# Kernel tuning notes

Hardware: AMD Instinct MI355X
Metric: run time of the kernel (lower is better)

Reference implementation:

```python
import jax, jax.numpy as jnp
import numpy as np

B, T, D, H = 1, 2048, 1024, 16
HS = D // H  # 64
FF = 4 * D   # 4096
EPS = 1e-6


def rmsnorm(x, w):
    xf = x.astype(jnp.float32)
    n = xf * jax.lax.rsqrt(jnp.mean(xf * xf, axis=-1, keepdims=True) + EPS)
    return n.astype(x.dtype) * w


def setup_inputs() -> dict:
    key = jax.random.key(0)
    ks = jax.random.split(key, 9)
    s = 0.02
    return {
        "x": jax.random.normal(ks[0], (B, T, D), jnp.float32),
        "Wq": jax.random.normal(ks[1], (H, D, HS), jnp.float32) * s,
        "Wk": jax.random.normal(ks[2], (H, D, HS), jnp.float32) * s,
        "Wv": jax.random.normal(ks[3], (H, D, HS), jnp.float32) * s,
        "Wproj": jax.random.normal(ks[4], (H * HS, D), jnp.float32) * s,
        "bproj": jnp.zeros((D,), jnp.float32),
        "W1": jax.random.normal(ks[5], (D, FF), jnp.float32) * s,
        "W2": jax.random.normal(ks[6], (FF, D), jnp.float32) * s,
        "g1": jnp.ones((D,), jnp.float32),
        "g2": jnp.ones((D,), jnp.float32),
    }


def reference(x, Wq, Wk, Wv, Wproj, bproj, W1, W2, g1, g2):
    # --- self attention on RMSNorm(x) ---
    xn = rmsnorm(x, g1)                                   # [B,T,D]
    q = jnp.einsum('btd,hds->bhts', xn, Wq)               # [B,H,T,hs]
    k = jnp.einsum('btd,hds->bhts', xn, Wk)
    v = jnp.einsum('btd,hds->bhts', xn, Wv)
    scale = HS ** -0.5
    wei = jnp.einsum('bhts,bhus->bhtu', q, k) * scale     # [B,H,T,T]
    causal = jnp.tril(jnp.ones((T, T), bool))
    wei = jnp.where(causal, wei, -jnp.inf)
    wei = jax.nn.softmax(wei, axis=-1)
    attn = jnp.einsum('bhtu,bhus->bhts', wei, v)          # [B,H,T,hs]
    attn = attn.transpose(0, 2, 1, 3).reshape(B, T, H * HS)
    sa = attn @ Wproj + bproj                             # [B,T,D]
    x = x + sa
    # --- SiLU FFN on RMSNorm(x) ---
    xn2 = rmsnorm(x, g2)
    h = jax.nn.silu(xn2 @ W1)                             # [B,T,4D]
    x = x + h @ W2
    return x
```

## Files before the change

### kernel.cpp

```cpp
#include <hip/hip_runtime.h>

typedef unsigned short u16;
typedef unsigned int u32;
typedef __attribute__((ext_vector_type(4))) float f32x4;
typedef __attribute__((ext_vector_type(8))) __bf16 bf16x8;

#define T_SEQ 2048
#define DMODEL 1024
#define NHEAD 16
#define HEADS 64
#define FFDIM 4096
#define MNQ 2097152l

__device__ __forceinline__ u16 f2bf(float f) {
  u32 u = __builtin_bit_cast(u32, f);
  u = u + 0x7FFFu + ((u >> 16) & 1u);
  return (u16)(u >> 16);
}
__device__ __forceinline__ float bf2f(u16 h) {
  u32 u = ((u32)h) << 16;
  return __builtin_bit_cast(float, u);
}
__device__ __forceinline__ void gload_lds16(const u16* g, u16* l) {
  __builtin_amdgcn_global_load_lds(
      (const __attribute__((address_space(1))) u32*)g,
      (__attribute__((address_space(3))) u32*)l, 16, 0, 0);
}

__global__ __launch_bounds__(256) void prep_k(
    const float* __restrict__ Wq, const float* __restrict__ Wk,
    const float* __restrict__ Wv, const float* __restrict__ Wproj,
    const float* __restrict__ W1, const float* __restrict__ W2,
    const float* __restrict__ x, const float* __restrict__ g1,
    u16* __restrict__ QKVwT, u16* __restrict__ WprojT,
    u16* __restrict__ W1T, u16* __restrict__ W2T, u16* __restrict__ xn1) {
  __shared__ u16 tile[64 * 66];
  __shared__ float wsum[4];
  int bid = blockIdx.x;
  int tid = threadIdx.x;
  if (bid >= 3072) {
    int row = bid - 3072;
    const float4* xr = (const float4*)(x + (long)row * DMODEL);
    float4 v = xr[tid];
    float ss = v.x * v.x + v.y * v.y + v.z * v.z + v.w * v.w;
#pragma unroll
    for (int off = 32; off >= 1; off >>= 1) ss += __shfl_xor(ss, off, 64);
    if ((tid & 63) == 0) wsum[tid >> 6] = ss;
    __syncthreads();
    float tot = wsum[0] + wsum[1] + wsum[2] + wsum[3];
    float rms = rsqrtf(tot * (1.0f / DMODEL) + 1e-6f);
    float4 gv = ((const float4*)g1)[tid];
    ushort4 o4 = make_ushort4(f2bf(v.x * rms * gv.x), f2bf(v.y * rms * gv.y),
                              f2bf(v.z * rms * gv.z), f2bf(v.w * rms * gv.w));
    ((ushort4*)(xn1 + (long)row * DMODEL))[tid] = o4;
    return;
  }
  const float* in;
  u16* out;
  long ldin, ldout;
  int r0, c0;
  if (bid < 768) {
    int z = bid >> 4, xi = bid & 15;
    int wsel = z >> 4, h = z & 15;
    in = (wsel == 0 ? Wq : (wsel == 1 ? Wk : Wv)) + (long)h * 65536;
    out = QKVwT + (long)wsel * 1048576 + (long)h * 65536;
    ldin = 64; ldout = 1024;
    r0 = xi * 64; c0 = 0;
  } else if (bid < 1024) {
    int b = bid - 768;
    in = Wproj; out = WprojT; ldin = 1024; ldout = 1024;
    r0 = (b >> 4) * 64; c0 = (b & 15) * 64;
  } else if (bid < 2048) {
    int b = bid - 1024;
    in = W1; out = W1T; ldin = 4096; ldout = 1024;
    r0 = (b & 15) * 64; c0 = (b >> 4) * 64;
  } else {
    int b = bid - 2048;
    in = W2; out = W2T; ldin = 1024; ldout = 4096;
    r0 = (b >> 4) * 64; c0 = (b & 15) * 64;
  }
#pragma unroll
  for (int p = 0; p < 16; ++p) {
    int idx = p * 256 + tid;
    int r = idx >> 6, c = idx & 63;
    tile[c * 66 + r] = f2bf(in[(long)(r0 + r) * ldin + c0 + c]);
  }
  __syncthreads();
#pragma unroll
  for (int p = 0; p < 16; ++p) {
    int idx = p * 256 + tid;
    int c = idx >> 6, r = idx & 63;
    out[(long)(c0 + c) * ldout + r0 + r] = tile[c * 66 + r];
  }
}

__global__ __launch_bounds__(256) void proj_rms_k(
    const u16* __restrict__ part, const float* __restrict__ bias,
    const float* __restrict__ resid, const float* __restrict__ g,
    float* __restrict__ x1, u16* __restrict__ xn2) {
  int row = blockIdx.x;
  int tid = threadIdx.x;
  long i = (long)row * DMODEL + tid * 4;
  float4 r = *(const float4*)(resid + i);
  float4 bi = *(const float4*)(bias + tid * 4);
  float4 v;
  v.x = r.x + bi.x; v.y = r.y + bi.y; v.z = r.z + bi.z; v.w = r.w + bi.w;
#pragma unroll
  for (int z = 0; z < 2; ++z) {
    ushort4 a = *(const ushort4*)(part + z * MNQ + i);
    v.x += bf2f(a.x); v.y += bf2f(a.y); v.z += bf2f(a.z); v.w += bf2f(a.w);
  }
  *(float4*)(x1 + i) = v;
  float ss = v.x * v.x + v.y * v.y + v.z * v.z + v.w * v.w;
#pragma unroll
  for (int off = 32; off >= 1; off >>= 1) ss += __shfl_xor(ss, off, 64);
  __shared__ float wsum[4];
  if ((tid & 63) == 0) wsum[tid >> 6] = ss;
  __syncthreads();
  float tot = wsum[0] + wsum[1] + wsum[2] + wsum[3];
  float rms = rsqrtf(tot * (1.0f / DMODEL) + 1e-6f);
  float4 gv = ((const float4*)g)[tid];
  ushort4 o4 = make_ushort4(f2bf(v.x * rms * gv.x), f2bf(v.y * rms * gv.y),
                            f2bf(v.z * rms * gv.z), f2bf(v.w * rms * gv.w));
  ((ushort4*)(xn2 + (long)row * DMODEL))[tid] = o4;
}

template <int EPI, int MODE, int NITER>
__global__ __launch_bounds__(256, 3) void gemm_bt_k(
    const u16* __restrict__ A, const u16* __restrict__ Bt, int N,
    u16* __restrict__ out16, u16* __restrict__ vt,
    u16* __restrict__ p0, u16* __restrict__ p1) {
  __shared__ __align__(16) u16 As[3][128 * 32];
  __shared__ __align__(16) u16 Bs[3][128 * 32];
  const int K = 1024 * ((EPI == 4 && MODE == 1) ? 4 : 1);
  const int kc = NITER * 32;
  int tid = threadIdx.x;
  int w = tid >> 6, lane = tid & 63;
  int quad = lane >> 4, l15 = lane & 15;
  int wr = w >> 1, wc = w & 1;

  int bid = blockIdx.x;
  int xcd = bid & 7, s = bid >> 3;
  int nn = N >> 7;
  int bx, by, kz;
  if (MODE == 0) {
    int nl = nn >> 3;
    by = xcd * nl + s % nl;
    int r = s / nl;
    bx = r & 15;
    kz = r >> 4;
  } else {
    bx = xcd * 2 + (s & 1);
    int r = s >> 1;
    by = r % nn;
    kz = r / nn;
  }
  int m0 = bx * 128, n0 = by * 128;

  f32x4 acc[4][4] = {};

  int lr = lane >> 2;
  int sw = (lr >> 1) & 3;
  int lc = ((lane & 3) ^ sw) * 8;
  const u16* Ak = A + (long)(m0 + w * 32 + lr) * K + lc + (long)kz * kc;
  const u16* A2k = Ak + (long)16 * K;
  const u16* Bk = Bt + (long)(n0 + w * 32 + lr) * K + lc + (long)kz * kc;
  const u16* B2k = Bk + (long)16 * K;

  gload_lds16(Ak, As[0] + w * 1024);
  gload_lds16(A2k, As[0] + w * 1024 + 512);
  gload_lds16(Bk, Bs[0] + w * 1024);
  gload_lds16(B2k, Bs[0] + w * 1024 + 512);
  gload_lds16(Ak + 32, As[1] + w * 1024);
  gload_lds16(A2k + 32, As[1] + w * 1024 + 512);
  gload_lds16(Bk + 32, Bs[1] + w * 1024);
  gload_lds16(B2k + 32, Bs[1] + w * 1024 + 512);

  int swq = (l15 >> 1) & 3;
  int qoff = (quad ^ swq) << 3;

#pragma unroll
  for (int k = 0; k < NITER; ++k) {
    const int cb = k % 3;
    if (k + 2 < NITER) {
      asm volatile("s_waitcnt vmcnt(4)\n\ts_barrier" ::: "memory");
      const int pb = (k + 2) % 3;
      const int off = (k + 2) * 32;
      gload_lds16(Ak + off, As[pb] + w * 1024);
      gload_lds16(A2k + off, As[pb] + w * 1024 + 512);
      gload_lds16(Bk + off, Bs[pb] + w * 1024);
      gload_lds16(B2k + off, Bs[pb] + w * 1024 + 512);
    } else {
      asm volatile("s_waitcnt vmcnt(0)\n\ts_barrier" ::: "memory");
    }
    const u16* Ab = As[cb];
    const u16* Bb = Bs[cb];
    bf16x8 af[4], bfr[4];
#pragma unroll
    for (int mt = 0; mt < 4; ++mt)
      af[mt] = *(const bf16x8*)(Ab + (wr * 64 + mt * 16 + l15) * 32 + qoff);
#pragma unroll
    for (int nt = 0; nt < 4; ++nt)
      bfr[nt] = *(const bf16x8*)(Bb + (wc * 64 + nt * 16 + l15) * 32 + qoff);
#pragma unroll
    for (int mt = 0; mt < 4; ++mt)
#pragma unroll
      for (int nt = 0; nt < 4; ++nt)
        acc[mt][nt] = __builtin_amdgcn_mfma_f32_16x16x32_bf16(
            af[mt], bfr[nt], acc[mt][nt], 0, 0, 0);
  }

  bool vblock = (EPI == 0) && (vt != nullptr) && (n0 >= 2048);
  u16* pb = nullptr;
  if (EPI == 4) pb = (kz < 4 ? p0 : p1) + (long)(kz & 3) * MNQ;
#pragma unroll
  for (int mt = 0; mt < 4; ++mt)
#pragma unroll
    for (int nt = 0; nt < 4; ++nt) {
      int col = n0 + wc * 64 + nt * 16 + l15;
      if (EPI == 0 && vblock) {
        int sc = col - 2048;
        int row0 = m0 + wr * 64 + mt * 16 + quad * 4;
        ushort4 pk = make_ushort4(f2bf(acc[mt][nt][0]), f2bf(acc[mt][nt][1]),
                                  f2bf(acc[mt][nt][2]), f2bf(acc[mt][nt][3]));
        *(ushort4*)(vt + (long)sc * 2048 + row0) = pk;
        continue;
      }
#pragma unroll
      for (int r = 0; r < 4; ++r) {
        int row = m0 + wr * 64 + mt * 16 + quad * 4 + r;
        long idx = (long)row * N + col;
        float v = acc[mt][nt][r];
        if (EPI == 0) {
          out16[idx] = f2bf(v);
        } else if (EPI == 2) {
          out16[idx] = f2bf(v / (1.0f + __expf(-v)));
        } else if (EPI == 4) {
          pb[idx] = f2bf(v);
        }
      }
    }
}

__global__ __launch_bounds__(256) void reduce_ffn2_k(
    const u16* __restrict__ p0, const u16* __restrict__ p1,
    const float* __restrict__ resid, float* __restrict__ out) {
  long i = ((long)blockIdx.x * 256 + threadIdx.x) * 4;
  float4 r = *(const float4*)(resid + i);
  float4 o = r;
#pragma unroll
  for (int z = 0; z < 4; ++z) {
    ushort4 a = *(const ushort4*)(p0 + z * MNQ + i);
    ushort4 b = *(const ushort4*)(p1 + z * MNQ + i);
    o.x += bf2f(a.x) + bf2f(b.x);
    o.y += bf2f(a.y) + bf2f(b.y);
    o.z += bf2f(a.z) + bf2f(b.z);
    o.w += bf2f(a.w) + bf2f(b.w);
  }
  *(float4*)(out + i) = o;
}

#define LSTR 72
__global__ __launch_bounds__(256) void attn_part_k(const u16* __restrict__ QKV,
                                                   const u16* __restrict__ Vt,
                                                   u16* __restrict__ Opart,
                                                   float* __restrict__ lpart,
                                                   u16* __restrict__ attn) {
  __shared__ __align__(16) u16 Qs[64 * LSTR];
  __shared__ __align__(16) u16 Ks[64 * LSTR];
  __shared__ __align__(16) u16 Vs[64 * LSTR];
  __shared__ float lbuf[64];

  int tid = threadIdx.x;
  int w = tid >> 6, lane = tid & 63;
  int quad = lane >> 4, l15 = lane & 15;

  int bid = blockIdx.x;
  int xcd = bid & 7, sg = bid >> 3;
  int h = xcd * 2 + (sg & 1);
  int p = sg >> 1;

  int bx = 0, acc0 = 0;
  while (true) {
    int n = (bx >> 3) + 1;
    if (p < acc0 + n) break;
    acc0 += n;
    ++bx;
  }
  int c = p - acc0;
  int t0 = bx * 64;
  int jstart = c * 8;
  int jend = min(jstart + 8, bx + 1);

#pragma unroll
  for (int pp = 0; pp < 2; ++pp) {
    int idx = pp * 256 + tid;
    int row = idx >> 3, cc = idx & 7;
    *(uint4*)(Qs + row * LSTR + cc * 8) =
        *(const uint4*)(QKV + (long)(t0 + row) * 3072 + h * 64 + cc * 8);
  }
  __syncthreads();
  bf16x8 aq[2];
#pragma unroll
  for (int ks = 0; ks < 2; ++ks)
    aq[ks] = *(const bf16x8*)(Qs + (w * 16 + l15) * LSTR + ks * 32 + quad * 8);

  f32x4 oacc[4] = {};
  float lsum = 0.f;
  int qg = t0 + w * 16 + l15;

  u16* PsW = Qs + w * (16 * LSTR);

  for (int j = jstart; j < jend; ++j) {
    __syncthreads();
#pragma unroll
    for (int pp = 0; pp < 2; ++pp) {
      int idx = pp * 256 + tid;
      int row = idx >> 3, cc = idx & 7;
      *(uint4*)(Ks + row * LSTR + cc * 8) =
          *(const uint4*)(QKV + (long)(j * 64 + row) * 3072 + 1024 + h * 64 + cc * 8);
      *(uint4*)(Vs + row * LSTR + cc * 8) =
          *(const uint4*)(Vt + (long)h * (64 * 2048) + (long)row * 2048 + j * 64 + cc * 8);
    }
    __syncthreads();

    f32x4 sacc[4] = {};
#pragma unroll
    for (int ks = 0; ks < 2; ++ks)
#pragma unroll
      for (int ut = 0; ut < 4; ++ut) {
        bf16x8 kf = *(const bf16x8*)(Ks + (ut * 16 + l15) * LSTR + ks * 32 + quad * 8);
        sacc[ut] = __builtin_amdgcn_mfma_f32_16x16x32_bf16(kf, aq[ks], sacc[ut], 0, 0, 0);
      }

    bool boundary = (j == bx);
#pragma unroll
    for (int ut = 0; ut < 4; ++ut) {
      float pv[4];
#pragma unroll
      for (int r = 0; r < 4; ++r) {
        float v = exp2f(sacc[ut][r] * 0.18033688f);
        if (boundary) {
          int u = j * 64 + ut * 16 + quad * 4 + r;
          if (u > qg) v = 0.f;
        }
        pv[r] = v;
        lsum += v;
      }
      ushort4 pk = make_ushort4(f2bf(pv[0]), f2bf(pv[1]), f2bf(pv[2]), f2bf(pv[3]));
      *(ushort4*)(PsW + l15 * LSTR + ut * 16 + quad * 4) = pk;
    }
    asm volatile("s_waitcnt lgkmcnt(0)" ::: "memory");
#pragma unroll
    for (int ks = 0; ks < 2; ++ks) {
      bf16x8 pf = *(const bf16x8*)(PsW + l15 * LSTR + ks * 32 + quad * 8);
#pragma unroll
      for (int ct = 0; ct < 4; ++ct) {
        bf16x8 vf = *(const bf16x8*)(Vs + (ct * 16 + l15) * LSTR + ks * 32 + quad * 8);
        oacc[ct] = __builtin_amdgcn_mfma_f32_16x16x32_bf16(pf, vf, oacc[ct], 0, 0, 0);
      }
    }
  }

  lsum += __shfl_xor(lsum, 16, 64);
  lsum += __shfl_xor(lsum, 32, 64);
  if (quad == 0) lbuf[w * 16 + l15] = 1.0f / lsum;
  asm volatile("s_waitcnt lgkmcnt(0)" ::: "memory");

  float inv[4];
#pragma unroll
  for (int r = 0; r < 4; ++r) inv[r] = lbuf[w * 16 + quad * 4 + r];

  if (bx < 8) {
#pragma unroll
    for (int ct = 0; ct < 4; ++ct)
#pragma unroll
      for (int r = 0; r < 4; ++r)
        attn[(long)(t0 + w * 16 + quad * 4 + r) * 1024 + h * 64 + ct * 16 + l15] =
            f2bf(oacc[ct][r] * inv[r]);
    return;
  }
  long slot = (long)p * 16 + h;
  u16* Ob = Opart + slot * 4096;
#pragma unroll
  for (int ct = 0; ct < 4; ++ct)
#pragma unroll
    for (int r = 0; r < 4; ++r)
      Ob[(w * 16 + quad * 4 + r) * 64 + ct * 16 + l15] = f2bf(oacc[ct][r] * inv[r]);
  if (quad == 0) lpart[slot * 64 + w * 16 + l15] = lsum;
}

__global__ __launch_bounds__(256) void attn_combine_k(
    const u16* __restrict__ Opart, const float* __restrict__ lpart,
    u16* __restrict__ out) {
  int bx = blockIdx.x + 8, h = blockIdx.y;
  int g = bx >> 3;
  int p0 = 4 * g * (g + 1) + (bx - 8 * g) * (g + 1);
  int nc = g + 1;
  int tid = threadIdx.x;
  int row = tid >> 2, c4 = (tid & 3) * 16;

  float lv[4];
  float wsum = 0.f;
  for (int cidx = 0; cidx < nc; ++cidx) {
    long slot = (long)(p0 + cidx) * 16 + h;
    lv[cidx] = lpart[slot * 64 + row];
    wsum += lv[cidx];
  }
  float rinv = 1.0f / wsum;

  float o[16];
#pragma unroll
  for (int i = 0; i < 16; ++i) o[i] = 0.f;
  for (int cidx = 0; cidx < nc; ++cidx) {
    float wc = lv[cidx] * rinv;
    const u16* Ob = Opart + ((long)(p0 + cidx) * 16 + h) * 4096 + row * 64 + c4;
    bf16x8 a = *(const bf16x8*)Ob;
    bf16x8 b = *(const bf16x8*)(Ob + 8);
#pragma unroll
    for (int i = 0; i < 8; ++i) {
      o[i] += wc * (float)a[i];
      o[8 + i] += wc * (float)b[i];
    }
  }
  u16 ob[16];
#pragma unroll
  for (int i = 0; i < 16; ++i) ob[i] = f2bf(o[i]);
  u16* op = out + (long)(bx * 64 + row) * 1024 + h * 64 + c4;
  *(uint4*)op = *(uint4*)ob;
  *(uint4*)(op + 8) = *(uint4*)(ob + 8);
}

extern "C" void kernel_launch(void* const* d_in, const int* in_sizes, int n_in,
                              void* d_out, int out_size, void* d_ws, size_t ws_size,
                              hipStream_t stream) {
  const float* x     = (const float*)d_in[0];
  const float* Wq    = (const float*)d_in[1];
  const float* Wk    = (const float*)d_in[2];
  const float* Wv    = (const float*)d_in[3];
  const float* Wproj = (const float*)d_in[4];
  const float* bproj = (const float*)d_in[5];
  const float* W1    = (const float*)d_in[6];
  const float* W2    = (const float*)d_in[7];
  const float* g1    = (const float*)d_in[8];
  const float* g2    = (const float*)d_in[9];

  char* ws = (char*)d_ws;
  u16* QKVwT  = (u16*)(ws);
  u16* WprojT = (u16*)(ws + (6ul << 20));
  u16* W1T    = (u16*)(ws + (8ul << 20));
  u16* W2T    = (u16*)(ws + (16ul << 20));
  u16* xn1    = (u16*)(ws + (24ul << 20));
  u16* QKVb   = (u16*)(ws + (28ul << 20));
  u16* VtB    = (u16*)(ws + (40ul << 20));
  u16* attn   = (u16*)(ws + (44ul << 20));
  float* x1   = (float*)(ws + (48ul << 20));
  u16* xn2    = (u16*)(ws + (56ul << 20));
  u16* hbuf   = (u16*)(ws + (60ul << 20));
  u16* Opart    = (u16*)(ws + (48ul << 20));
  float* lpart  = (float*)(ws + (58ul << 20));
  u16* projp    = (u16*)(ws + (28ul << 20));
  u16* ffn2pA   = (u16*)(ws + (28ul << 20));
  u16* ffn2pB   = (u16*)(ws);
  if (ws_size < (76ul << 20)) return;

  dim3 blk(256);

  prep_k<<<dim3(5120), blk, 0, stream>>>(
      Wq, Wk, Wv, Wproj, W1, W2, x, g1, QKVwT, WprojT, W1T, W2T, xn1);
  gemm_bt_k<0, 0, 32><<<dim3(384), blk, 0, stream>>>(
      xn1, QKVwT, 3072, QKVb, VtB, nullptr, nullptr);
  attn_part_k<<<dim3(1280), blk, 0, stream>>>(QKVb, VtB, Opart, lpart, attn);
  attn_combine_k<<<dim3(24, 16), blk, 0, stream>>>(Opart, lpart, attn);
  gemm_bt_k<4, 0, 16><<<dim3(256), blk, 0, stream>>>(
      attn, WprojT, 1024, nullptr, nullptr, projp, nullptr);
  proj_rms_k<<<dim3(2048), blk, 0, stream>>>(projp, bproj, x, g2, x1, xn2);
  gemm_bt_k<2, 0, 32><<<dim3(512), blk, 0, stream>>>(
      xn2, W1T, 4096, hbuf, nullptr, nullptr, nullptr);
  gemm_bt_k<4, 1, 16><<<dim3(1024), blk, 0, stream>>>(
      hbuf, W2T, 1024, nullptr, nullptr, ffn2pA, ffn2pB);
  reduce_ffn2_k<<<dim3(2048), blk, 0, stream>>>(ffn2pA, ffn2pB, x1, (float*)d_out);
}
```

Before: 249.7 us.

## Overlap W1/W2 transposes with QKV GEMM, vectorize transposes, halve FFN2 split-K

The W1/W2 fp32-to-bf16 transposes move out of the prep kernel and run as extra fill blocks inside the QKV GEMM launch, so they can overlap with the GEMM's tail. The transpose helper now uses float4 loads and 16-byte stores instead of scalar accesses. The FFN2 GEMM goes from 8 split-K partials to 4 (NITER 32, 512 blocks), which cuts partial-buffer traffic and the reduce work at the cost of fewer blocks in flight. A risk is that the fill blocks compete for LDS and CUs with the GEMM blocks.

```diff
diff --git a/kernel.cpp b/kernel.cpp
--- a/kernel.cpp
+++ b/kernel.cpp
@@ -27,19 +27,43 @@
       (__attribute__((address_space(3))) u32*)l, 16, 0, 0);
 }
 
+__device__ __forceinline__ void transpose64(const float* __restrict__ in,
+                                            long ldin, u16* __restrict__ out,
+                                            long ldout, int r0, int c0, int tid,
+                                            u16* tile) {
+#pragma unroll
+  for (int p = 0; p < 4; ++p) {
+    int idx = p * 256 + tid;
+    int r = idx >> 4, c4 = (idx & 15) * 4;
+    float4 v = *(const float4*)(in + (long)(r0 + r) * ldin + c0 + c4);
+    tile[(c4 + 0) * 66 + r] = f2bf(v.x);
+    tile[(c4 + 1) * 66 + r] = f2bf(v.y);
+    tile[(c4 + 2) * 66 + r] = f2bf(v.z);
+    tile[(c4 + 3) * 66 + r] = f2bf(v.w);
+  }
+  __syncthreads();
+#pragma unroll
+  for (int p = 0; p < 2; ++p) {
+    int idx = p * 256 + tid;
+    int c = idx >> 3, rg = (idx & 7) * 8;
+    u16 tmp[8];
+#pragma unroll
+    for (int j = 0; j < 8; ++j) tmp[j] = tile[c * 66 + rg + j];
+    *(uint4*)(out + (long)(c0 + c) * ldout + r0 + rg) = *(uint4*)tmp;
+  }
+}
+
 __global__ __launch_bounds__(256) void prep_k(
     const float* __restrict__ Wq, const float* __restrict__ Wk,
     const float* __restrict__ Wv, const float* __restrict__ Wproj,
-    const float* __restrict__ W1, const float* __restrict__ W2,
     const float* __restrict__ x, const float* __restrict__ g1,
-    u16* __restrict__ QKVwT, u16* __restrict__ WprojT,
-    u16* __restrict__ W1T, u16* __restrict__ W2T, u16* __restrict__ xn1) {
+    u16* __restrict__ QKVwT, u16* __restrict__ WprojT, u16* __restrict__ xn1) {
   __shared__ u16 tile[64 * 66];
   __shared__ float wsum[4];
   int bid = blockIdx.x;
   int tid = threadIdx.x;
-  if (bid >= 3072) {
-    int row = bid - 3072;
+  if (bid >= 1024) {
+    int row = bid - 1024;
     const float4* xr = (const float4*)(x + (long)row * DMODEL);
     float4 v = xr[tid];
     float ss = v.x * v.x + v.y * v.y + v.z * v.z + v.w * v.w;
@@ -66,32 +90,12 @@
     out = QKVwT + (long)wsel * 1048576 + (long)h * 65536;
     ldin = 64; ldout = 1024;
     r0 = xi * 64; c0 = 0;
-  } else if (bid < 1024) {
+  } else {
     int b = bid - 768;
     in = Wproj; out = WprojT; ldin = 1024; ldout = 1024;
     r0 = (b >> 4) * 64; c0 = (b & 15) * 64;
-  } else if (bid < 2048) {
-    int b = bid - 1024;
-    in = W1; out = W1T; ldin = 4096; ldout = 1024;
-    r0 = (b & 15) * 64; c0 = (b >> 4) * 64;
-  } else {
-    int b = bid - 2048;
-    in = W2; out = W2T; ldin = 1024; ldout = 4096;
-    r0 = (b >> 4) * 64; c0 = (b & 15) * 64;
-  }
-#pragma unroll
-  for (int p = 0; p < 16; ++p) {
-    int idx = p * 256 + tid;
-    int r = idx >> 6, c = idx & 63;
-    tile[c * 66 + r] = f2bf(in[(long)(r0 + r) * ldin + c0 + c]);
-  }
-  __syncthreads();
-#pragma unroll
-  for (int p = 0; p < 16; ++p) {
-    int idx = p * 256 + tid;
-    int c = idx >> 6, r = idx & 63;
-    out[(long)(c0 + c) * ldout + r0 + r] = tile[c * 66 + r];
-  }
+  }
+  transpose64(in, ldin, out, ldout, r0, c0, tid, tile);
 }
 
 __global__ __launch_bounds__(256) void proj_rms_k(
@@ -125,13 +129,35 @@
   ((ushort4*)(xn2 + (long)row * DMODEL))[tid] = o4;
 }
 
-template <int EPI, int MODE, int NITER>
+template <int EPI, int MODE, int NITER, bool FILL = false>
 __global__ __launch_bounds__(256, 3) void gemm_bt_k(
     const u16* __restrict__ A, const u16* __restrict__ Bt, int N,
     u16* __restrict__ out16, u16* __restrict__ vt,
-    u16* __restrict__ p0, u16* __restrict__ p1) {
+    u16* __restrict__ p0, u16* __restrict__ p1,
+    const float* __restrict__ F1, const float* __restrict__ F2,
+    u16* __restrict__ FT1, u16* __restrict__ FT2, int ngemm) {
   __shared__ __align__(16) u16 As[3][128 * 32];
   __shared__ __align__(16) u16 Bs[3][128 * 32];
+  if constexpr (FILL) {
+    if ((int)blockIdx.x >= ngemm) {
+      int tb = (int)blockIdx.x - ngemm;
+      u16* tile = (u16*)As;
+      const float* in;
+      u16* out;
+      long ldin, ldout;
+      int r0, c0;
+      if (tb < 1024) {
+        in = F1; out = FT1; ldin = 4096; ldout = 1024;
+        r0 = (tb & 15) * 64; c0 = (tb >> 4) * 64;
+      } else {
+        int b = tb - 1024;
+        in = F2; out = FT2; ldin = 1024; ldout = 4096;
+        r0 = (b >> 4) * 64; c0 = (b & 15) * 64;
+      }
+      transpose64(in, ldin, out, ldout, r0, c0, threadIdx.x, tile);
+      return;
+    }
+  }
   const int K = 1024 * ((EPI == 4 && MODE == 1) ? 4 : 1);
   const int kc = NITER * 32;
   int tid = threadIdx.x;
@@ -243,19 +269,18 @@
 }
 
 __global__ __launch_bounds__(256) void reduce_ffn2_k(
-    const u16* __restrict__ p0, const u16* __restrict__ p1,
-    const float* __restrict__ resid, float* __restrict__ out) {
+    const u16* __restrict__ p0, const float* __restrict__ resid,
+    float* __restrict__ out) {
   long i = ((long)blockIdx.x * 256 + threadIdx.x) * 4;
   float4 r = *(const float4*)(resid + i);
   float4 o = r;
 #pragma unroll
   for (int z = 0; z < 4; ++z) {
     ushort4 a = *(const ushort4*)(p0 + z * MNQ + i);
-    ushort4 b = *(const ushort4*)(p1 + z * MNQ + i);
-    o.x += bf2f(a.x) + bf2f(b.x);
-    o.y += bf2f(a.y) + bf2f(b.y);
-    o.z += bf2f(a.z) + bf2f(b.z);
-    o.w += bf2f(a.w) + bf2f(b.w);
+    o.x += bf2f(a.x);
+    o.y += bf2f(a.y);
+    o.z += bf2f(a.z);
+    o.w += bf2f(a.w);
   }
   *(float4*)(out + i) = o;
 }
@@ -460,24 +485,26 @@
   u16* Opart    = (u16*)(ws + (48ul << 20));
   float* lpart  = (float*)(ws + (58ul << 20));
   u16* projp    = (u16*)(ws + (28ul << 20));
-  u16* ffn2pA   = (u16*)(ws + (28ul << 20));
-  u16* ffn2pB   = (u16*)(ws);
+  u16* ffn2p    = (u16*)(ws + (28ul << 20));
   if (ws_size < (76ul << 20)) return;
 
   dim3 blk(256);
 
-  prep_k<<<dim3(5120), blk, 0, stream>>>(
-      Wq, Wk, Wv, Wproj, W1, W2, x, g1, QKVwT, WprojT, W1T, W2T, xn1);
-  gemm_bt_k<0, 0, 32><<<dim3(384), blk, 0, stream>>>(
-      xn1, QKVwT, 3072, QKVb, VtB, nullptr, nullptr);
+  prep_k<<<dim3(3072), blk, 0, stream>>>(
+      Wq, Wk, Wv, Wproj, x, g1, QKVwT, WprojT, xn1);
+  gemm_bt_k<0, 0, 32, true><<<dim3(2432), blk, 0, stream>>>(
+      xn1, QKVwT, 3072, QKVb, VtB, nullptr, nullptr, W1, W2, W1T, W2T, 384);
   attn_part_k<<<dim3(1280), blk, 0, stream>>>(QKVb, VtB, Opart, lpart, attn);
   attn_combine_k<<<dim3(24, 16), blk, 0, stream>>>(Opart, lpart, attn);
   gemm_bt_k<4, 0, 16><<<dim3(256), blk, 0, stream>>>(
-      attn, WprojT, 1024, nullptr, nullptr, projp, nullptr);
+      attn, WprojT, 1024, nullptr, nullptr, projp, nullptr,
+      nullptr, nullptr, nullptr, nullptr, 0);
   proj_rms_k<<<dim3(2048), blk, 0, stream>>>(projp, bproj, x, g2, x1, xn2);
   gemm_bt_k<2, 0, 32><<<dim3(512), blk, 0, stream>>>(
-      xn2, W1T, 4096, hbuf, nullptr, nullptr, nullptr);
-  gemm_bt_k<4, 1, 16><<<dim3(1024), blk, 0, stream>>>(
-      hbuf, W2T, 1024, nullptr, nullptr, ffn2pA, ffn2pB);
-  reduce_ffn2_k<<<dim3(2048), blk, 0, stream>>>(ffn2pA, ffn2pB, x1, (float*)d_out);
-}
+      xn2, W1T, 4096, hbuf, nullptr, nullptr, nullptr,
+      nullptr, nullptr, nullptr, nullptr, 0);
+  gemm_bt_k<4, 1, 32><<<dim3(512), blk, 0, stream>>>(
+      hbuf, W2T, 1024, nullptr, nullptr, ffn2p, nullptr,
+      nullptr, nullptr, nullptr, nullptr, 0);
+  reduce_ffn2_k<<<dim3(2048), blk, 0, stream>>>(ffn2p, x1, (float*)d_out);
+}
```

Result: faster. 244.5 us (-2.1%).
